# Kernel tuning notes

Hardware: AMD Instinct MI355X
Metric: run time of the kernel (lower is better)

Reference implementation:

```python
import jax, jax.numpy as jnp
import numpy as np


def haar_level(x):
    """One 2D Haar (periodization-equivalent for even sizes) DWT on [B,K,C,H,W].
    Returns [B,4K,C,H/2,W/2] with per-parent band order (LL, Hx, Hy, Hxy),
    matching the tree's append order yl, yh0, yh1, yh2."""
    B, K, C, H, W = x.shape
    x = x.reshape(B, K, C, H // 2, 2, W // 2, 2)
    a = x[:, :, :, :, 0, :, 0]
    b = x[:, :, :, :, 0, :, 1]
    c = x[:, :, :, :, 1, :, 0]
    d = x[:, :, :, :, 1, :, 1]
    ll = (a + b + c + d) * 0.5
    h1 = (a - b + c - d) * 0.5   # high along width
    h2 = (a + b - c - d) * 0.5   # high along height
    h3 = (a - b - c + d) * 0.5   # diagonal
    out = jnp.stack([ll, h1, h2, h3], axis=2)  # [B,K,4,C,H/2,W/2]
    return out.reshape(B, 4 * K, C, H // 2, W // 2)


def conv2d(x, w, b, stride, pad):
    y = jax.lax.conv_general_dilated(
        x, w, window_strides=(stride, stride),
        padding=[(pad, pad), (pad, pad)],
        dimension_numbers=('NCHW', 'OIHW', 'NCHW'))
    return y + b[None, :, None, None]


def setup_inputs() -> dict:
    key = jax.random.key(0)
    ks = jax.random.split(key, 9)
    s = 0.05
    return {
        'x':        jax.random.normal(ks[0], (64, 3, 224, 224), dtype=jnp.float32),
        'w_s1':     jax.random.normal(ks[1], (192, 3, 7, 7), dtype=jnp.float32) * s,
        'b_s1':     jax.random.normal(ks[2], (192,), dtype=jnp.float32) * s,
        'w_s2':     jax.random.normal(ks[3], (192, 192, 7, 7), dtype=jnp.float32) * s,
        'b_s2':     jax.random.normal(ks[4], (192,), dtype=jnp.float32) * s,
        'w_p':      jax.random.normal(ks[5], (768, 960, 3, 3), dtype=jnp.float32) * s,
        'b_p':      jax.random.normal(ks[6], (768,), dtype=jnp.float32) * s,
        'cls_token': jax.random.normal(ks[7], (1, 1, 768), dtype=jnp.float32),
        'positions': jax.random.normal(ks[8], (50, 768), dtype=jnp.float32),
    }


def reference(x, w_s1, b_s1, w_s2, b_s2, w_p, b_p, cls_token, positions):
    B = x.shape[0]
    # ---- 4-level full Haar wavelet packet tree (vectorized over subbands) ----
    t = x[:, None]                      # [B,1,3,224,224]
    for _ in range(4):
        t = haar_level(t)               # -> [B,256,3,14,14]
    wav = t.reshape(B, 256 * 3, 14, 14)  # [B,768,14,14] (tree concat order)
    # ---- spatial branch: two strided 7x7 convs (224 -> 56 -> 14) ----
    sp = conv2d(x, w_s1, b_s1, stride=4, pad=3)
    sp = conv2d(sp, w_s2, b_s2, stride=4, pad=3)   # [B,192,14,14]
    feat = jnp.concatenate([wav, sp], axis=1)      # [B,960,14,14]
    # ---- patch projection conv 3x3 s2 -> 7x7, flatten to tokens ----
    y = conv2d(feat, w_p, b_p, stride=2, pad=1)    # [B,768,7,7]
    y = y.reshape(B, 768, 49).transpose(0, 2, 1)   # [B,49,768]
    cls = jnp.broadcast_to(cls_token, (B, 1, 768))
    y = jnp.concatenate([cls, y], axis=1) + positions  # [B,50,768]
    return y
```

## Files before the change

### kernel.cpp

```cpp
#include <hip/hip_runtime.h>
#include <stdint.h>

typedef __attribute__((ext_vector_type(8))) short short8;
typedef __attribute__((ext_vector_type(4))) float floatx4;

__device__ inline unsigned short f2bf(float f){
  union { float fv; unsigned int u; } v; v.fv = f;
  unsigned int u = v.u;
  unsigned int r = ((u >> 16) & 1u) + 0x7FFFu;
  return (unsigned short)((u + r) >> 16);
}

__device__ __forceinline__ void async16(const void* g, void* l){
  __builtin_amdgcn_global_load_lds(
      (const __attribute__((address_space(1))) unsigned int*)g,
      (__attribute__((address_space(3))) unsigned int*)l, 16, 0, 0);
}

__global__ void prep_w1(const float* __restrict__ w, unsigned short* __restrict__ w1p){
  int i = blockIdx.x*256 + threadIdx.x;
  if (i >= 192*192) return;
  int k = i % 192, o = i / 192;
  int cc = k >> 3, kx = k & 7;
  unsigned short v = 0;
  if (cc < 21 && kx < 7){
    int c = cc / 7, ky = cc % 7;
    v = f2bf(w[(o*3 + c)*49 + ky*7 + kx]);
  }
  w1p[i] = v;
}
__global__ void prep_w2(const float* __restrict__ w, unsigned short* __restrict__ w2p){
  int i = blockIdx.x*256 + threadIdx.x;
  if (i >= 192*9408) return;
  int k = i % 9408, o = i / 9408;
  int g = k / 192, c = k % 192;
  int ky = g / 7, kx = g % 7;
  w2p[i] = f2bf(w[((o*192 + c)*7 + ky)*7 + kx]);
}
__global__ void prep_w3(const float* __restrict__ w, unsigned short* __restrict__ w3p){
  int i = blockIdx.x*256 + threadIdx.x;
  if (i >= 768*8640) return;
  int k = i % 8640, o = i / 8640;
  int g = k / 960, c = k % 960;
  int ky = g / 3, kx = g % 3;
  w3p[i] = f2bf(w[((o*960 + c)*3 + ky)*3 + kx]);
}
__global__ void prep_zp(unsigned int* __restrict__ zp){
  zp[threadIdx.x] = 0u;
}

__global__ void pad_x(const float* __restrict__ x, unsigned short* __restrict__ xh){
  int idx = blockIdx.x*256 + threadIdx.x;
  if (idx >= 64*3*230*232) return;
  int px = idx % 232; int t = idx / 232;
  int py = t % 230;   t /= 230;
  unsigned short v = 0;
  if (py >= 3 && py < 227 && px >= 3 && px < 227)
    v = f2bf(x[((size_t)t*224 + (py-3))*224 + (px-3)]);
  xh[idx] = v;
}

__global__ void wavelet_kernel(const float* __restrict__ x, unsigned short* __restrict__ feat){
  int blk = blockIdx.x;
  int j = blk % 14; blk /= 14;
  int i = blk % 14; blk /= 14;
  int c = blk % 3;  int b = blk / 3;
  int t = threadIdx.x;
  int u = t >> 4, v = t & 15;
  float val = x[((size_t)(b*3 + c)*224 + (i*16 + u))*224 + (j*16 + v)];
  #pragma unroll
  for (int bit = 1; bit < 64; bit <<= 1){
    float p = __shfl_xor(val, bit);
    val = (t & bit) ? (p - val) : (val + p);
  }
  __shared__ float s[256];
  #pragma unroll
  for (int bit = 64; bit < 256; bit <<= 1){
    s[t] = val; __syncthreads();
    float p = s[t ^ bit]; __syncthreads();
    val = (t & bit) ? (p - val) : (val + p);
  }
  s[t] = val; __syncthreads();
  int k = t;
  int d1 = (k>>6)&3, d2 = (k>>4)&3, d3 = (k>>2)&3, d4 = k&3;
  int mr = (d1>>1) | ((d2>>1)<<1) | ((d3>>1)<<2) | ((d4>>1)<<3);
  int mc = (d1&1)  | ((d2&1)<<1)  | ((d3&1)<<2)  | ((d4&1)<<3);
  float outv = s[mr*16 + mc] * 0.0625f;
  feat[((size_t)((b*14 + i)*14 + j))*960 + (k*3 + c)] = f2bf(outv);
}

__global__ __launch_bounds__(256) void conv1_gemm(const unsigned short* __restrict__ xh,
                                                  const unsigned short* __restrict__ w1p,
                                                  const float* __restrict__ b1,
                                                  unsigned short* __restrict__ sp1){
  constexpr int LDK = 200;
  __shared__ unsigned short As[64*LDK], Bs[64*LDK];
  int m0 = blockIdx.x*64, n0 = blockIdx.y*64;
  int tid = threadIdx.x;
  #pragma unroll
  for (int i = 0; i < 6; i++){
    int id = tid + i*256; int row = id/24, cc = id%24;
    *(uint4*)&Bs[row*LDK + cc*8] = *(const uint4*)&w1p[(n0+row)*192 + cc*8];
  }
  #pragma unroll
  for (int i = 0; i < 6; i++){
    int id = tid + i*256; int row = id/24, cc = id%24;
    int m = m0 + row; int ox = m % 56; int t = m / 56; int oy = t % 56; int b = t / 56;
    uint2 v0 = make_uint2(0u,0u), v1 = v0;
    if (cc < 21){
      int c = cc / 7, ky = cc % 7;
      const unsigned short* p = xh + ((size_t)((b*3 + c)*230 + 4*oy + ky))*232 + 4*ox;
      v0 = *(const uint2*)p;
      v1 = *(const uint2*)(p + 4);
    }
    *(uint2*)&As[row*LDK + cc*8]     = v0;
    *(uint2*)&As[row*LDK + cc*8 + 4] = v1;
  }
  __syncthreads();
  int lane = tid & 63, wave = tid >> 6;
  int l16 = lane & 15, quad = lane >> 4;
  int wy = wave >> 1, wx = wave & 1;
  floatx4 acc[2][2];
  #pragma unroll
  for (int a = 0; a < 2; a++)
    #pragma unroll
    for (int bq = 0; bq < 2; bq++) acc[a][bq] = (floatx4){0.f,0.f,0.f,0.f};
  #pragma unroll
  for (int ks = 0; ks < 6; ks++){
    short8 a0 = *(const short8*)&As[(wy*32      + l16)*LDK + ks*32 + quad*8];
    short8 a1 = *(const short8*)&As[(wy*32 + 16 + l16)*LDK + ks*32 + quad*8];
    short8 b0 = *(const short8*)&Bs[(wx*32      + l16)*LDK + ks*32 + quad*8];
    short8 b1 = *(const short8*)&Bs[(wx*32 + 16 + l16)*LDK + ks*32 + quad*8];
    acc[0][0] = __builtin_amdgcn_mfma_f32_16x16x32_bf16(a0, b0, acc[0][0], 0, 0, 0);
    acc[0][1] = __builtin_amdgcn_mfma_f32_16x16x32_bf16(a0, b1, acc[0][1], 0, 0, 0);
    acc[1][0] = __builtin_amdgcn_mfma_f32_16x16x32_bf16(a1, b0, acc[1][0], 0, 0, 0);
    acc[1][1] = __builtin_amdgcn_mfma_f32_16x16x32_bf16(a1, b1, acc[1][1], 0, 0, 0);
  }
  #pragma unroll
  for (int mt = 0; mt < 2; mt++){
    #pragma unroll
    for (int rg = 0; rg < 4; rg++){
      int row = wy*32 + mt*16 + quad*4 + rg;
      int mm = m0 + row;
      int ox = mm % 56; int t2 = mm / 56; int oy = t2 % 56; int bb = t2 / 56;
      size_t obase = ((size_t)((bb*56 + oy)*56 + ox))*192;
      #pragma unroll
      for (int nt = 0; nt < 2; nt++){
        int nn = n0 + wx*32 + nt*16 + l16;
        sp1[obase + nn] = f2bf(acc[mt][nt][rg] + b1[nn]);
      }
    }
  }
}

template<int MODE>
__global__ __launch_bounds__(256) void conv_gemm(const unsigned short* __restrict__ Ain,
                                                 const unsigned short* __restrict__ Bt,
                                                 const float* __restrict__ bias,
                                                 const float* __restrict__ pos,
                                                 const unsigned short* __restrict__ zp,
                                                 void* __restrict__ outp){
  constexpr int OH  = (MODE==2) ? 14 : 7;
  constexpr int OW  = OH;
  constexpr int IH  = (MODE==2) ? 56 : 14;
  constexpr int IW  = IH;
  constexpr int Cin = (MODE==2) ? 192 : 960;
  constexpr int KW  = (MODE==2) ? 7 : 3;
  constexpr int S   = (MODE==2) ? 4 : 2;
  constexpr int P   = (MODE==2) ? 3 : 1;
  constexpr int K   = (MODE==2) ? 9408 : 8640;
  constexpr int MTI = (MODE==2) ? 196 : 49;
  constexpr int GRP = (MODE==2) ? 24 : 96;

  int id = blockIdx.x;
  int g = id / GRP, rem = id % GRP;
  int mtile = g*8 + (rem & 7), ntile = rem >> 3;
  if (mtile >= MTI) return;
  int m0 = mtile*64, n0 = ntile*64;

  __shared__ unsigned short As[64*64], Bs[64*64];
  int tid = threadIdx.x, wave = tid >> 6, lane = tid & 63;
  int l16 = lane & 15, quad = lane >> 4;
  int wy = wave >> 1, wx = wave & 1;

  int r8 = lane >> 3, kb7 = lane & 7;
  int kb = kb7 ^ r8;
  int rA0 = wave*16 + r8, rA1 = rA0 + 8;

  int m_0 = m0 + rA0;
  int ox0 = m_0 % OW; int t0 = m_0 / OW; int oy0 = t0 % OH; int bb0 = t0 / OH;
  int iyb0 = S*oy0 - P, ixb0 = S*ox0 - P;
  int abase0 = ((bb0*IH + iyb0)*IW + ixb0)*Cin + kb*8;
  int m_1 = m0 + rA1;
  int ox1 = m_1 % OW; int t1 = m_1 / OW; int oy1 = t1 % OH; int bb1 = t1 / OH;
  int iyb1 = S*oy1 - P, ixb1 = S*ox1 - P;
  int abase1 = ((bb1*IH + iyb1)*IW + ixb1)*Cin + kb*8;

  const unsigned short* pB0 = Bt + (size_t)(n0 + rA0)*K + kb*8;
  const unsigned short* pB1 = Bt + (size_t)(n0 + rA1)*K + kb*8;

  void* dA0 = (void*)&As[(wave*16    )*64];
  void* dA1 = (void*)&As[(wave*16 + 8)*64];
  void* dB0 = (void*)&Bs[(wave*16    )*64];
  void* dB1 = (void*)&Bs[(wave*16 + 8)*64];

  int sw = l16 & 7;
  int x0 = ((0 + quad) ^ sw) * 8;
  int x1 = ((4 + quad) ^ sw) * 8;
  int aoff0 = (wy*32      + l16)*64;
  int aoff1 = (wy*32 + 16 + l16)*64;
  int boff0 = (wx*32      + l16)*64;
  int boff1 = (wx*32 + 16 + l16)*64;

  floatx4 acc[2][2];
  #pragma unroll
  for (int a = 0; a < 2; a++)
    #pragma unroll
    for (int bq = 0; bq < 2; bq++) acc[a][bq] = (floatx4){0.f,0.f,0.f,0.f};

  int c0 = 0, ky = 0, kx = 0;
  for (int k0 = 0; k0 < K; k0 += 64){
    int koff = (ky*IW + kx)*Cin + c0;
    int iy0 = iyb0 + ky, ix0 = ixb0 + kx;
    int iy1 = iyb1 + ky, ix1 = ixb1 + kx;
    const unsigned short* pa0 = ((unsigned)iy0 < (unsigned)IH && (unsigned)ix0 < (unsigned)IW)
                                ? (Ain + (abase0 + koff)) : zp;
    const unsigned short* pa1 = ((unsigned)iy1 < (unsigned)IH && (unsigned)ix1 < (unsigned)IW)
                                ? (Ain + (abase1 + koff)) : zp;
    __syncthreads();
    async16(pa0, dA0);
    async16(pa1, dA1);
    async16(pB0 + k0, dB0);
    async16(pB1 + k0, dB1);
    __syncthreads();

    #pragma unroll
    for (int ks = 0; ks < 2; ks++){
      int xo = ks ? x1 : x0;
      short8 a0 = *(const short8*)&As[aoff0 + xo];
      short8 a1 = *(const short8*)&As[aoff1 + xo];
      short8 b0 = *(const short8*)&Bs[boff0 + xo];
      short8 b1 = *(const short8*)&Bs[boff1 + xo];
      acc[0][0] = __builtin_amdgcn_mfma_f32_16x16x32_bf16(a0, b0, acc[0][0], 0, 0, 0);
      acc[0][1] = __builtin_amdgcn_mfma_f32_16x16x32_bf16(a0, b1, acc[0][1], 0, 0, 0);
      acc[1][0] = __builtin_amdgcn_mfma_f32_16x16x32_bf16(a1, b0, acc[1][0], 0, 0, 0);
      acc[1][1] = __builtin_amdgcn_mfma_f32_16x16x32_bf16(a1, b1, acc[1][1], 0, 0, 0);
    }

    c0 += 64;
    if (c0 == Cin){ c0 = 0; kx++; if (kx == KW){ kx = 0; ky++; } }
  }

  #pragma unroll
  for (int mt = 0; mt < 2; mt++){
    #pragma unroll
    for (int rg = 0; rg < 4; rg++){
      int row = wy*32 + mt*16 + quad*4 + rg;
      int mm = m0 + row;
      int ox2 = mm % OW; int t2 = mm / OW; int oy2 = t2 % OH; int bb2 = t2 / OH;
      #pragma unroll
      for (int nt = 0; nt < 2; nt++){
        int nn = n0 + wx*32 + nt*16 + l16;
        float v = acc[mt][nt][rg] + bias[nn];
        if (MODE == 2){
          ((unsigned short*)outp)[((size_t)((bb2*14 + oy2)*14 + ox2))*960 + 768 + nn] = f2bf(v);
        } else {
          int tt = oy2*7 + ox2;
          v += pos[(size_t)(1 + tt)*768 + nn];
          ((float*)outp)[((size_t)(bb2*50 + 1 + tt))*768 + nn] = v;
        }
      }
    }
  }
}

__global__ void cls_kernel(const float* __restrict__ cls, const float* __restrict__ pos,
                           float* __restrict__ out){
  int i = blockIdx.x*256 + threadIdx.x;
  if (i >= 64*768) return;
  int e = i % 768, b = i / 768;
  out[(size_t)(b*50)*768 + e] = cls[e] + pos[e];
}

extern "C" void kernel_launch(void* const* d_in, const int* in_sizes, int n_in,
                              void* d_out, int out_size, void* d_ws, size_t ws_size,
                              hipStream_t stream){
  (void)in_sizes; (void)n_in; (void)out_size;
  const float* x    = (const float*)d_in[0];
  const float* w_s1 = (const float*)d_in[1];
  const float* b_s1 = (const float*)d_in[2];
  const float* w_s2 = (const float*)d_in[3];
  const float* b_s2 = (const float*)d_in[4];
  const float* w_p  = (const float*)d_in[5];
  const float* b_p  = (const float*)d_in[6];
  const float* cls  = (const float*)d_in[7];
  const float* pos  = (const float*)d_in[8];
  float* out = (float*)d_out;

  char* ws = (char*)d_ws;
  if (ws_size < 119504896u) return;
  unsigned short* w1p  = (unsigned short*)(ws + 0);
  unsigned short* w2p  = (unsigned short*)(ws + 131072);
  unsigned short* w3p  = (unsigned short*)(ws + 4194304);
  unsigned short* sp1  = (unsigned short*)(ws + 17825792);
  unsigned short* zp   = (unsigned short*)(ws + 94896128);
  unsigned short* feat = (unsigned short*)(ws + 95420416);
  unsigned short* xh   = feat;

  prep_w1<<<(192*192 + 255)/256, 256, 0, stream>>>(w_s1, w1p);
  prep_w2<<<(192*9408 + 255)/256, 256, 0, stream>>>(w_s2, w2p);
  prep_w3<<<(768*8640 + 255)/256, 256, 0, stream>>>(w_p, w3p);
  prep_zp<<<1, 64, 0, stream>>>((unsigned int*)zp);
  pad_x<<<(64*3*230*232)/256, 256, 0, stream>>>(x, xh);
  conv1_gemm<<<dim3(3136, 3), 256, 0, stream>>>(xh, w1p, b_s1, sp1);
  wavelet_kernel<<<64*3*14*14, 256, 0, stream>>>(x, feat);
  conv_gemm<2><<<600, 256, 0, stream>>>(sp1, w2p, b_s2, nullptr, zp, (void*)feat);
  conv_gemm<3><<<672, 256, 0, stream>>>(feat, w3p, b_p, pos, zp, (void*)out);
  cls_kernel<<<(64*768 + 255)/256, 256, 0, stream>>>(cls, pos, out);
}
```

Before: 429.0 us.

## Double-buffer conv GEMM K-loops and rework conv1 with im2col-friendly padded layout

The conv GEMM kernels now double-buffer their LDS tiles so the async global-to-LDS loads for the next K-step are issued while MFMAs run on the current step, leaving one barrier per iteration instead of two. conv1 is restructured: the padded input is pre-expanded into per-output-column 8-wide windows (pad_x2), which allows 16-byte async loads. It uses 128x64 tiles with a 3-stage pipelined K loop. The workspace layout is reshuffled so the expanded input aliases the w2p/w3p region, with the weight prep kernels moved after conv1. Epilogue index math is simplified.

```diff
diff --git a/kernel.cpp b/kernel.cpp
--- a/kernel.cpp
+++ b/kernel.cpp
@@ -49,15 +49,18 @@
   zp[threadIdx.x] = 0u;
 }
 
-__global__ void pad_x(const float* __restrict__ x, unsigned short* __restrict__ xh){
+__global__ void pad_x2(const float* __restrict__ x, unsigned short* __restrict__ xh2){
   int idx = blockIdx.x*256 + threadIdx.x;
-  if (idx >= 64*3*230*232) return;
-  int px = idx % 232; int t = idx / 232;
-  int py = t % 230;   t /= 230;
+  if (idx >= 64*3*230*56*8) return;
+  int kx = idx & 7; int t = idx >> 3;
+  int ox = t % 56;  t /= 56;
+  int iy = t % 230; t /= 230;
+  int row = iy - 3;
+  int col = 4*ox - 3 + kx;
   unsigned short v = 0;
-  if (py >= 3 && py < 227 && px >= 3 && px < 227)
-    v = f2bf(x[((size_t)t*224 + (py-3))*224 + (px-3)]);
-  xh[idx] = v;
+  if (row >= 0 && row < 224 && col >= 0 && col < 224)
+    v = f2bf(x[((size_t)t*224 + row)*224 + col]);
+  xh2[idx] = v;
 }
 
 __global__ void wavelet_kernel(const float* __restrict__ x, unsigned short* __restrict__ feat){
@@ -89,65 +92,85 @@
   feat[((size_t)((b*14 + i)*14 + j))*960 + (k*3 + c)] = f2bf(outv);
 }
 
-__global__ __launch_bounds__(256) void conv1_gemm(const unsigned short* __restrict__ xh,
+__global__ __launch_bounds__(256) void conv1_gemm(const unsigned short* __restrict__ xh2,
                                                   const unsigned short* __restrict__ w1p,
                                                   const float* __restrict__ b1,
                                                   unsigned short* __restrict__ sp1){
-  constexpr int LDK = 200;
-  __shared__ unsigned short As[64*LDK], Bs[64*LDK];
-  int m0 = blockIdx.x*64, n0 = blockIdx.y*64;
-  int tid = threadIdx.x;
-  #pragma unroll
-  for (int i = 0; i < 6; i++){
-    int id = tid + i*256; int row = id/24, cc = id%24;
-    *(uint4*)&Bs[row*LDK + cc*8] = *(const uint4*)&w1p[(n0+row)*192 + cc*8];
-  }
-  #pragma unroll
-  for (int i = 0; i < 6; i++){
-    int id = tid + i*256; int row = id/24, cc = id%24;
-    int m = m0 + row; int ox = m % 56; int t = m / 56; int oy = t % 56; int b = t / 56;
-    uint2 v0 = make_uint2(0u,0u), v1 = v0;
-    if (cc < 21){
-      int c = cc / 7, ky = cc % 7;
-      const unsigned short* p = xh + ((size_t)((b*3 + c)*230 + 4*oy + ky))*232 + 4*ox;
-      v0 = *(const uint2*)p;
-      v1 = *(const uint2*)(p + 4);
-    }
-    *(uint2*)&As[row*LDK + cc*8]     = v0;
-    *(uint2*)&As[row*LDK + cc*8 + 4] = v1;
-  }
-  __syncthreads();
-  int lane = tid & 63, wave = tid >> 6;
+  __shared__ unsigned short As[2][128*64], Bs[2][64*64];
+  int m0 = blockIdx.x*128, n0 = blockIdx.y*64;
+  int tid = threadIdx.x, wave = tid >> 6, lane = tid & 63;
   int l16 = lane & 15, quad = lane >> 4;
   int wy = wave >> 1, wx = wave & 1;
-  floatx4 acc[2][2];
-  #pragma unroll
-  for (int a = 0; a < 2; a++)
-    #pragma unroll
-    for (int bq = 0; bq < 2; bq++) acc[a][bq] = (floatx4){0.f,0.f,0.f,0.f};
-  #pragma unroll
-  for (int ks = 0; ks < 6; ks++){
-    short8 a0 = *(const short8*)&As[(wy*32      + l16)*LDK + ks*32 + quad*8];
-    short8 a1 = *(const short8*)&As[(wy*32 + 16 + l16)*LDK + ks*32 + quad*8];
-    short8 b0 = *(const short8*)&Bs[(wx*32      + l16)*LDK + ks*32 + quad*8];
-    short8 b1 = *(const short8*)&Bs[(wx*32 + 16 + l16)*LDK + ks*32 + quad*8];
-    acc[0][0] = __builtin_amdgcn_mfma_f32_16x16x32_bf16(a0, b0, acc[0][0], 0, 0, 0);
-    acc[0][1] = __builtin_amdgcn_mfma_f32_16x16x32_bf16(a0, b1, acc[0][1], 0, 0, 0);
-    acc[1][0] = __builtin_amdgcn_mfma_f32_16x16x32_bf16(a1, b0, acc[1][0], 0, 0, 0);
-    acc[1][1] = __builtin_amdgcn_mfma_f32_16x16x32_bf16(a1, b1, acc[1][1], 0, 0, 0);
-  }
-  #pragma unroll
-  for (int mt = 0; mt < 2; mt++){
+  int r8 = lane >> 3, kb = (lane & 7) ^ r8;
+
+  int Abase[4];
+  #pragma unroll
+  for (int j = 0; j < 4; j++){
+    int row = wave*32 + j*8 + r8;
+    int m = m0 + row;
+    int ox = m % 56; int t = m / 56; int oy = t % 56; int b = t / 56;
+    Abase[j] = (b*690 + 4*oy)*448 + ox*8;
+  }
+  const unsigned short* pB0 = w1p + (n0 + wave*16 + r8)*192 + kb*8;
+  const unsigned short* pB1 = pB0 + 8*192;
+
+  int sw = l16 & 7;
+  int xo0 = ((quad    ) ^ sw)*8;
+  int xo1 = ((quad + 4) ^ sw)*8;
+  int aoff[4];
+  #pragma unroll
+  for (int mt = 0; mt < 4; mt++) aoff[mt] = (wy*64 + mt*16 + l16)*64;
+  int boff0 = (wx*32 + l16)*64, boff1 = boff0 + 16*64;
+
+  floatx4 acc[4][2];
+  #pragma unroll
+  for (int mt = 0; mt < 4; mt++)
+    #pragma unroll
+    for (int nt = 0; nt < 2; nt++) acc[mt][nt] = (floatx4){0.f,0.f,0.f,0.f};
+
+  auto stage = [&](int i, int buf){
+    int cc = i*8 + kb;
+    int c = (cc*147) >> 10;
+    int ky = cc - 7*c;
+    int koff = (c*230 + ky)*448;
+    #pragma unroll
+    for (int j = 0; j < 4; j++)
+      async16(xh2 + Abase[j] + koff, (void*)&As[buf][(wave*32 + j*8)*64]);
+    async16(pB0 + i*64, (void*)&Bs[buf][(wave*16    )*64]);
+    async16(pB1 + i*64, (void*)&Bs[buf][(wave*16 + 8)*64]);
+  };
+
+  stage(0, 0);
+  __syncthreads();
+  #pragma unroll
+  for (int i = 0; i < 3; i++){
+    int buf = i & 1;
+    if (i < 2) stage(i+1, buf ^ 1);
+    #pragma unroll
+    for (int ks = 0; ks < 2; ks++){
+      int xo = ks ? xo1 : xo0;
+      short8 b0 = *(const short8*)&Bs[buf][boff0 + xo];
+      short8 b1 = *(const short8*)&Bs[buf][boff1 + xo];
+      #pragma unroll
+      for (int mt = 0; mt < 4; mt++){
+        short8 a = *(const short8*)&As[buf][aoff[mt] + xo];
+        acc[mt][0] = __builtin_amdgcn_mfma_f32_16x16x32_bf16(a, b0, acc[mt][0], 0, 0, 0);
+        acc[mt][1] = __builtin_amdgcn_mfma_f32_16x16x32_bf16(a, b1, acc[mt][1], 0, 0, 0);
+      }
+    }
+    __syncthreads();
+  }
+
+  #pragma unroll
+  for (int mt = 0; mt < 4; mt++){
     #pragma unroll
     for (int rg = 0; rg < 4; rg++){
-      int row = wy*32 + mt*16 + quad*4 + rg;
-      int mm = m0 + row;
-      int ox = mm % 56; int t2 = mm / 56; int oy = t2 % 56; int bb = t2 / 56;
-      size_t obase = ((size_t)((bb*56 + oy)*56 + ox))*192;
+      int row = wy*64 + mt*16 + quad*4 + rg;
+      size_t ob = (size_t)(m0 + row)*192;
       #pragma unroll
       for (int nt = 0; nt < 2; nt++){
         int nn = n0 + wx*32 + nt*16 + l16;
-        sp1[obase + nn] = f2bf(acc[mt][nt][rg] + b1[nn]);
+        sp1[ob + nn] = f2bf(acc[mt][nt][rg] + b1[nn]);
       }
     }
   }
@@ -169,6 +192,7 @@
   constexpr int S   = (MODE==2) ? 4 : 2;
   constexpr int P   = (MODE==2) ? 3 : 1;
   constexpr int K   = (MODE==2) ? 9408 : 8640;
+  constexpr int NIT = K/64;
   constexpr int MTI = (MODE==2) ? 196 : 49;
   constexpr int GRP = (MODE==2) ? 24 : 96;
 
@@ -178,13 +202,12 @@
   if (mtile >= MTI) return;
   int m0 = mtile*64, n0 = ntile*64;
 
-  __shared__ unsigned short As[64*64], Bs[64*64];
+  __shared__ unsigned short As[2][64*64], Bs[2][64*64];
   int tid = threadIdx.x, wave = tid >> 6, lane = tid & 63;
   int l16 = lane & 15, quad = lane >> 4;
   int wy = wave >> 1, wx = wave & 1;
 
-  int r8 = lane >> 3, kb7 = lane & 7;
-  int kb = kb7 ^ r8;
+  int r8 = lane >> 3, kb = (lane & 7) ^ r8;
   int rA0 = wave*16 + r8, rA1 = rA0 + 8;
 
   int m_0 = m0 + rA0;
@@ -199,14 +222,9 @@
   const unsigned short* pB0 = Bt + (size_t)(n0 + rA0)*K + kb*8;
   const unsigned short* pB1 = Bt + (size_t)(n0 + rA1)*K + kb*8;
 
-  void* dA0 = (void*)&As[(wave*16    )*64];
-  void* dA1 = (void*)&As[(wave*16 + 8)*64];
-  void* dB0 = (void*)&Bs[(wave*16    )*64];
-  void* dB1 = (void*)&Bs[(wave*16 + 8)*64];
-
   int sw = l16 & 7;
-  int x0 = ((0 + quad) ^ sw) * 8;
-  int x1 = ((4 + quad) ^ sw) * 8;
+  int xo0 = ((quad    ) ^ sw)*8;
+  int xo1 = ((quad + 4) ^ sw)*8;
   int aoff0 = (wy*32      + l16)*64;
   int aoff1 = (wy*32 + 16 + l16)*64;
   int boff0 = (wx*32      + l16)*64;
@@ -218,8 +236,9 @@
     #pragma unroll
     for (int bq = 0; bq < 2; bq++) acc[a][bq] = (floatx4){0.f,0.f,0.f,0.f};
 
-  int c0 = 0, ky = 0, kx = 0;
-  for (int k0 = 0; k0 < K; k0 += 64){
+  int c0 = 0, ky = 0, kx = 0, k0n = 0;
+
+  auto stage = [&](int buf){
     int koff = (ky*IW + kx)*Cin + c0;
     int iy0 = iyb0 + ky, ix0 = ixb0 + kx;
     int iy1 = iyb1 + ky, ix1 = ixb1 + kx;
@@ -227,28 +246,33 @@
                                 ? (Ain + (abase0 + koff)) : zp;
     const unsigned short* pa1 = ((unsigned)iy1 < (unsigned)IH && (unsigned)ix1 < (unsigned)IW)
                                 ? (Ain + (abase1 + koff)) : zp;
-    __syncthreads();
-    async16(pa0, dA0);
-    async16(pa1, dA1);
-    async16(pB0 + k0, dB0);
-    async16(pB1 + k0, dB1);
-    __syncthreads();
-
+    async16(pa0, (void*)&As[buf][(wave*16    )*64]);
+    async16(pa1, (void*)&As[buf][(wave*16 + 8)*64]);
+    async16(pB0 + k0n, (void*)&Bs[buf][(wave*16    )*64]);
+    async16(pB1 + k0n, (void*)&Bs[buf][(wave*16 + 8)*64]);
+    k0n += 64;
+    c0 += 64;
+    if (c0 == Cin){ c0 = 0; kx++; if (kx == KW){ kx = 0; ky++; } }
+  };
+
+  stage(0);
+  __syncthreads();
+  for (int i = 0; i < NIT; i++){
+    int buf = i & 1;
+    if (i + 1 < NIT) stage(buf ^ 1);
     #pragma unroll
     for (int ks = 0; ks < 2; ks++){
-      int xo = ks ? x1 : x0;
-      short8 a0 = *(const short8*)&As[aoff0 + xo];
-      short8 a1 = *(const short8*)&As[aoff1 + xo];
-      short8 b0 = *(const short8*)&Bs[boff0 + xo];
-      short8 b1 = *(const short8*)&Bs[boff1 + xo];
+      int xo = ks ? xo1 : xo0;
+      short8 a0 = *(const short8*)&As[buf][aoff0 + xo];
+      short8 a1 = *(const short8*)&As[buf][aoff1 + xo];
+      short8 b0 = *(const short8*)&Bs[buf][boff0 + xo];
+      short8 b1 = *(const short8*)&Bs[buf][boff1 + xo];
       acc[0][0] = __builtin_amdgcn_mfma_f32_16x16x32_bf16(a0, b0, acc[0][0], 0, 0, 0);
       acc[0][1] = __builtin_amdgcn_mfma_f32_16x16x32_bf16(a0, b1, acc[0][1], 0, 0, 0);
       acc[1][0] = __builtin_amdgcn_mfma_f32_16x16x32_bf16(a1, b0, acc[1][0], 0, 0, 0);
       acc[1][1] = __builtin_amdgcn_mfma_f32_16x16x32_bf16(a1, b1, acc[1][1], 0, 0, 0);
     }
-
-    c0 += 64;
-    if (c0 == Cin){ c0 = 0; kx++; if (kx == KW){ kx = 0; ky++; } }
+    __syncthreads();
   }
 
   #pragma unroll
@@ -257,17 +281,17 @@
     for (int rg = 0; rg < 4; rg++){
       int row = wy*32 + mt*16 + quad*4 + rg;
       int mm = m0 + row;
-      int ox2 = mm % OW; int t2 = mm / OW; int oy2 = t2 % OH; int bb2 = t2 / OH;
       #pragma unroll
       for (int nt = 0; nt < 2; nt++){
         int nn = n0 + wx*32 + nt*16 + l16;
         float v = acc[mt][nt][rg] + bias[nn];
         if (MODE == 2){
-          ((unsigned short*)outp)[((size_t)((bb2*14 + oy2)*14 + ox2))*960 + 768 + nn] = f2bf(v);
+          ((unsigned short*)outp)[(size_t)mm*960 + 768 + nn] = f2bf(v);
         } else {
-          int tt = oy2*7 + ox2;
+          int b2 = mm / 49;
+          int tt = mm - b2*49;
           v += pos[(size_t)(1 + tt)*768 + nn];
-          ((float*)outp)[((size_t)(bb2*50 + 1 + tt))*768 + nn] = v;
+          ((float*)outp)[((size_t)(mm + b2 + 1))*768 + nn] = v;
         }
       }
     }
@@ -298,21 +322,21 @@
   float* out = (float*)d_out;
 
   char* ws = (char*)d_ws;
-  if (ws_size < 119504896u) return;
+  if (ws_size < 118235136u) return;
   unsigned short* w1p  = (unsigned short*)(ws + 0);
-  unsigned short* w2p  = (unsigned short*)(ws + 131072);
-  unsigned short* w3p  = (unsigned short*)(ws + 4194304);
-  unsigned short* sp1  = (unsigned short*)(ws + 17825792);
-  unsigned short* zp   = (unsigned short*)(ws + 94896128);
-  unsigned short* feat = (unsigned short*)(ws + 95420416);
-  unsigned short* xh   = feat;
+  unsigned short* sp1  = (unsigned short*)(ws + 131072);
+  unsigned short* zp   = (unsigned short*)(ws + 77201408u);
+  unsigned short* w2p  = (unsigned short*)(ws + 77266944u);
+  unsigned short* w3p  = (unsigned short*)(ws + 80879616u);
+  unsigned short* feat = (unsigned short*)(ws + 94150656u);
+  unsigned short* xh2  = (unsigned short*)(ws + 77266944u);
 
   prep_w1<<<(192*192 + 255)/256, 256, 0, stream>>>(w_s1, w1p);
+  pad_x2<<<(64*3*230*56*8)/256, 256, 0, stream>>>(x, xh2);
+  conv1_gemm<<<dim3(1568, 3), 256, 0, stream>>>(xh2, w1p, b_s1, sp1);
   prep_w2<<<(192*9408 + 255)/256, 256, 0, stream>>>(w_s2, w2p);
   prep_w3<<<(768*8640 + 255)/256, 256, 0, stream>>>(w_p, w3p);
   prep_zp<<<1, 64, 0, stream>>>((unsigned int*)zp);
-  pad_x<<<(64*3*230*232)/256, 256, 0, stream>>>(x, xh);
-  conv1_gemm<<<dim3(3136, 3), 256, 0, stream>>>(xh, w1p, b_s1, sp1);
   wavelet_kernel<<<64*3*14*14, 256, 0, stream>>>(x, feat);
   conv_gemm<2><<<600, 256, 0, stream>>>(sp1, w2p, b_s2, nullptr, zp, (void*)feat);
   conv_gemm<3><<<672, 256, 0, stream>>>(feat, w3p, b_p, pos, zp, (void*)out);
```

Result: no change. 434.6 us (+1.3%).
